# Performance work log

Hardware: AMD Instinct MI355X
Metric: run time of the kernel (lower is better)

Reference implementation:

```python
import jax, jax.numpy as jnp
import numpy as np

N, CH, H, W = 8, 256, 64, 64
M, K = 4, 256
CG = CH // M  # per-group input channels


def setup_inputs() -> dict:
    key = jax.random.key(0)
    k1, k2 = jax.random.split(key)
    x = jax.random.normal(k1, (N, CH, H, W), dtype=jnp.float32)
    # grouped conv1x1 weight: [m, k, c_g]  (torch layout is [m*k, c_g, 1, 1])
    w = jax.random.normal(k2, (M, K, CG), dtype=jnp.float32) / np.float32(np.sqrt(CG))
    return {"x": x, "w": w}


def reference(x, w):
    n, c, h, wd = x.shape
    m, k, cg = w.shape
    # grouped 1x1 conv == per-group matmul over channels
    xg = x.reshape(n, m, cg, h, wd)
    logit5 = jnp.einsum('nmchw,mkc->nmhwk', xg, w)  # [n, m, h, w, k]
    # OneHotCategoricalStraightThrough.rsample():
    # hard one-hot sample + (probs - stop_grad(probs))
    probs = jax.nn.softmax(logit5, axis=-1)
    idx = jax.random.categorical(jax.random.key(42), logit5, axis=-1)  # [n, m, h, w]
    one_hot = jax.nn.one_hot(idx, k, dtype=logit5.dtype)
    quantized = jax.lax.stop_gradient(one_hot) + probs - jax.lax.stop_gradient(probs)
    code = jnp.argmax(quantized, axis=-1)  # [n, m, h, w]
    q_out = jnp.transpose(quantized, (0, 1, 4, 2, 3)).reshape(n, m * k, h, wd)
    logit = jnp.transpose(logit5, (0, 1, 4, 2, 3)).reshape(n, m * k, h, wd)
    return q_out, code, logit
```

## Files before the change

### kernel.cpp

```cpp
#include <hip/hip_runtime.h>
#include <stdint.h>

#define CODE_OFF  33554432u
#define LOGIT_OFF 33685504u

typedef __attribute__((address_space(1))) const void g_void;
typedef __attribute__((address_space(3))) void l_void;

__device__ __forceinline__ uint32_t rotl32(uint32_t x, int r) {
  return (x << r) | (x >> (32 - r));
}

__device__ __forceinline__ uint32_t tf32_part(uint32_t i) {
  const uint32_t ks1 = 42u;
  const uint32_t ks2 = 0x1BD11BDAu ^ 42u;
  uint32_t x0 = 0u;
  uint32_t x1 = i + ks1;
#define R4(a,b,c,d) \
  x0 += x1; x1 = rotl32(x1,(a)); x1 ^= x0; \
  x0 += x1; x1 = rotl32(x1,(b)); x1 ^= x0; \
  x0 += x1; x1 = rotl32(x1,(c)); x1 ^= x0; \
  x0 += x1; x1 = rotl32(x1,(d)); x1 ^= x0;
  R4(13,15,26,6)   x0 += ks1; x1 += ks2 + 1u;
  R4(17,29,16,24)  x0 += ks2; x1 += 2u;
  R4(13,15,26,6)               x1 += ks1 + 3u;
  R4(17,29,16,24)  x0 += ks1; x1 += ks2 + 4u;
  R4(13,15,26,6)   x0 += ks2; x1 += 5u;
#undef R4
  return x0 ^ x1;
}

__device__ __forceinline__ float bits_to_gumbel(uint32_t bits) {
  uint32_t fb = (bits >> 9) | 0x3f800000u;
  float f = __uint_as_float(fb) - 1.0f;
  float u = (f > 0.0f) ? f : 1.17549435e-38f;
  return -logf(-logf(u));
}

__global__ __launch_bounds__(256, 4)
void mcq_kernel(const float* __restrict__ x, const float* __restrict__ w,
                float* __restrict__ out) {
  __shared__ __align__(16) float x_lds[2048];
  __shared__ __align__(16) float w_lds[4096];

  const int tid = threadIdx.x;
  const int tx = tid & 7;
  const int ty = tid >> 3;
  const int half = tx >> 2;
  const int px = tx & 3;
  const int bid = blockIdx.x;
  const int nm = bid >> 8;
  const int tile = bid & 255;
  const int hw0 = tile * 16;
  const int n = nm >> 2;
  const int m = nm & 3;

  float* q_out = out;
  float* code_out = out + CODE_OFF;
  float* logit_out = out + LOGIT_OFF;

  {
    const float* xA = x + (size_t)(n * 256 + m * 64) * 4096 + hw0;
    const float* xB = xA + (size_t)4 * 256 * 4096;
#pragma unroll
    for (int it = 0; it < 2; ++it) {
      int idx = it * 256 + tid;
      int c = idx >> 3;
      int hs = (idx >> 2) & 1;
      int ck = idx & 3;
      const float* src = (hs ? xB : xA) + (size_t)c * 4096 + ck * 4;
      float* dst = x_lds + ((it * 256 + (tid & ~63)) << 2);
      __builtin_amdgcn_global_load_lds((g_void*)src, (l_void*)dst, 16, 0, 0);
    }
  }

  const float* wrow = w + (size_t)m * 256 * 64;
  float4 wr0, wr1;
  {
    const float* wk = wrow + tid * 64;
    wr0 = *(const float4*)(wk + 0);
    wr1 = *(const float4*)(wk + 4);
    w_lds[0 * 256 + tid] = wr0.x; w_lds[1 * 256 + tid] = wr0.y;
    w_lds[2 * 256 + tid] = wr0.z; w_lds[3 * 256 + tid] = wr0.w;
    w_lds[4 * 256 + tid] = wr1.x; w_lds[5 * 256 + tid] = wr1.y;
    w_lds[6 * 256 + tid] = wr1.z; w_lds[7 * 256 + tid] = wr1.w;
  }
  __syncthreads();

  float acc0[8], acc1[8], acc2[8], acc3[8];
  float gmb0[8], gmb1[8], gmb2[8], gmb3[8];
#pragma unroll
  for (int i = 0; i < 8; ++i) acc0[i] = acc1[i] = acc2[i] = acc3[i] = 0.0f;

  const uint32_t base0 = ((uint32_t)((nm + 16 * half) * 4096 + hw0 + 4 * px)) << 8;

#pragma unroll
  for (int chunk = 0; chunk < 8; ++chunk) {
    if (chunk < 7) {
      const float* wk = wrow + tid * 64 + (chunk + 1) * 8;
      wr0 = *(const float4*)(wk + 0);
      wr1 = *(const float4*)(wk + 4);
    }
    {
      const uint32_t k = (uint32_t)((chunk >> 2) * 128 + ty * 4 + (chunk & 3));
      uint32_t b0 = tf32_part(base0 + 0u * 256u + k);
      uint32_t b1 = tf32_part(base0 + 1u * 256u + k);
      uint32_t b2 = tf32_part(base0 + 2u * 256u + k);
      uint32_t b3 = tf32_part(base0 + 3u * 256u + k);
      gmb0[chunk] = bits_to_gumbel(b0);
      gmb1[chunk] = bits_to_gumbel(b1);
      gmb2[chunk] = bits_to_gumbel(b2);
      gmb3[chunk] = bits_to_gumbel(b3);
    }
    const int rb = (chunk & 1) * 2048;
#pragma unroll
    for (int cc = 0; cc < 8; ++cc) {
      int c = chunk * 8 + cc;
      float4 xv = *(const float4*)&x_lds[c * 32 + half * 16 + px * 4];
      float wv[8];
      *(float4*)&wv[0] = *(const float4*)&w_lds[rb + cc * 256 +   0 + ty * 4];
      *(float4*)&wv[4] = *(const float4*)&w_lds[rb + cc * 256 + 128 + ty * 4];
#pragma unroll
      for (int jd = 0; jd < 8; ++jd) {
        float wkv = wv[jd];
        acc0[jd] += xv.x * wkv;
        acc1[jd] += xv.y * wkv;
        acc2[jd] += xv.z * wkv;
        acc3[jd] += xv.w * wkv;
      }
    }
    if (chunk < 7) {
      const int wb = ((chunk + 1) & 1) * 2048;
      w_lds[wb + 0 * 256 + tid] = wr0.x; w_lds[wb + 1 * 256 + tid] = wr0.y;
      w_lds[wb + 2 * 256 + tid] = wr0.z; w_lds[wb + 3 * 256 + tid] = wr0.w;
      w_lds[wb + 4 * 256 + tid] = wr1.x; w_lds[wb + 5 * 256 + tid] = wr1.y;
      w_lds[wb + 6 * 256 + tid] = wr1.z; w_lds[wb + 7 * 256 + tid] = wr1.w;
      __syncthreads();
    }
  }

  float best0 = -3.4e38f, best1 = -3.4e38f, best2 = -3.4e38f, best3 = -3.4e38f;
  int i0 = 0, i1 = 0, i2 = 0, i3 = 0;
  const size_t row_off = (size_t)hw0 + 4 * px;
#pragma unroll
  for (int jd = 0; jd < 8; ++jd) {
    int k = (jd >> 2) * 128 + ty * 4 + (jd & 3);
    size_t off = (size_t)((nm + 16 * half) * 256 + k) * 4096 + row_off;
    *(float4*)(logit_out + off) = make_float4(acc0[jd], acc1[jd], acc2[jd], acc3[jd]);
    float v0 = gmb0[jd] + acc0[jd];
    float v1 = gmb1[jd] + acc1[jd];
    float v2 = gmb2[jd] + acc2[jd];
    float v3 = gmb3[jd] + acc3[jd];
    if (v0 > best0) { best0 = v0; i0 = k; }
    if (v1 > best1) { best1 = v1; i1 = k; }
    if (v2 > best2) { best2 = v2; i2 = k; }
    if (v3 > best3) { best3 = v3; i3 = k; }
  }

  __syncthreads();
  float* red_val = x_lds;
  int* red_idx = (int*)w_lds;
  {
    int slot = half * 16 + px * 4;
    red_val[(slot + 0) * 33 + ty] = best0;  red_idx[(slot + 0) * 33 + ty] = i0;
    red_val[(slot + 1) * 33 + ty] = best1;  red_idx[(slot + 1) * 33 + ty] = i1;
    red_val[(slot + 2) * 33 + ty] = best2;  red_idx[(slot + 2) * 33 + ty] = i2;
    red_val[(slot + 3) * 33 + ty] = best3;  red_idx[(slot + 3) * 33 + ty] = i3;
  }
  __syncthreads();
  int* idx_final = (int*)(x_lds + 1088);
  if (tid < 32) {
    float bv = -3.4e38f; int bi = 0x7fffffff;
#pragma unroll
    for (int t2 = 0; t2 < 32; ++t2) {
      float v = red_val[tid * 33 + t2];
      int ix = red_idx[tid * 33 + t2];
      if (v > bv || (v == bv && ix < bi)) { bv = v; bi = ix; }
    }
    idx_final[tid] = bi;
    int h = tid >> 4;
    int pos = tid & 15;
    code_out[(size_t)(nm + 16 * h) * 4096 + hw0 + pos] = (float)bi;
  }
  __syncthreads();

  const int f0 = idx_final[half * 16 + px * 4 + 0];
  const int f1 = idx_final[half * 16 + px * 4 + 1];
  const int f2 = idx_final[half * 16 + px * 4 + 2];
  const int f3 = idx_final[half * 16 + px * 4 + 3];
#pragma unroll
  for (int jd = 0; jd < 8; ++jd) {
    int k = (jd >> 2) * 128 + ty * 4 + (jd & 3);
    size_t off = (size_t)((nm + 16 * half) * 256 + k) * 4096 + row_off;
    *(float4*)(q_out + off) = make_float4(k == f0 ? 1.0f : 0.0f, k == f1 ? 1.0f : 0.0f,
                                          k == f2 ? 1.0f : 0.0f, k == f3 ? 1.0f : 0.0f);
  }
}

extern "C" void kernel_launch(void* const* d_in, const int* in_sizes, int n_in,
                              void* d_out, int out_size, void* d_ws, size_t ws_size,
                              hipStream_t stream) {
  const float* x = (const float*)d_in[0];
  const float* w = (const float*)d_in[1];
  float* out = (float*)d_out;
  mcq_kernel<<<dim3(4096), dim3(256), 0, stream>>>(x, w, out);
}
```

Measured before the change: 382.7 us.

## Split each block to one plane, doubling grid and halving per-thread tile

Each block now handles a single (n,m) plane instead of two, so the grid doubles to 8192 blocks and each thread computes a 4x4 tile instead of 4x8. The x tile in LDS is halved, Gumbel noise per thread is halved, and the argmax reduction becomes a two-stage 16-slot reduction over 64 threads per pixel. The goal is lower register pressure and more parallelism to hide memory latency in this store-bound kernel. The cost is that every weight slice is loaded and transposed into LDS twice as often overall, and there are extra barriers.

Result: slower. 406.4 us (+6.2%).

```diff
diff --git a/kernel.cpp b/kernel.cpp
--- a/kernel.cpp
+++ b/kernel.cpp
@@ -40,38 +40,29 @@
 __global__ __launch_bounds__(256, 4)
 void mcq_kernel(const float* __restrict__ x, const float* __restrict__ w,
                 float* __restrict__ out) {
-  __shared__ __align__(16) float x_lds[2048];
+  __shared__ __align__(16) float x_lds[1024];
   __shared__ __align__(16) float w_lds[4096];
 
   const int tid = threadIdx.x;
-  const int tx = tid & 7;
-  const int ty = tid >> 3;
-  const int half = tx >> 2;
-  const int px = tx & 3;
+  const int px = tid & 3;
+  const int ty = tid >> 2;
   const int bid = blockIdx.x;
-  const int nm = bid >> 8;
+  const int nm = bid >> 9;
+  const int half = (bid >> 8) & 1;
   const int tile = bid & 255;
   const int hw0 = tile * 16;
-  const int n = nm >> 2;
   const int m = nm & 3;
+  const int plane = nm + 16 * half;
 
   float* q_out = out;
   float* code_out = out + CODE_OFF;
   float* logit_out = out + LOGIT_OFF;
 
   {
-    const float* xA = x + (size_t)(n * 256 + m * 64) * 4096 + hw0;
-    const float* xB = xA + (size_t)4 * 256 * 4096;
-#pragma unroll
-    for (int it = 0; it < 2; ++it) {
-      int idx = it * 256 + tid;
-      int c = idx >> 3;
-      int hs = (idx >> 2) & 1;
-      int ck = idx & 3;
-      const float* src = (hs ? xB : xA) + (size_t)c * 4096 + ck * 4;
-      float* dst = x_lds + ((it * 256 + (tid & ~63)) << 2);
-      __builtin_amdgcn_global_load_lds((g_void*)src, (l_void*)dst, 16, 0, 0);
-    }
+    const float* xbase = x + (size_t)plane * 262144 + hw0;
+    const float* src = xbase + (size_t)(tid >> 2) * 4096 + (tid & 3) * 4;
+    float* dst = x_lds + ((tid & ~63) << 2);
+    __builtin_amdgcn_global_load_lds((g_void*)src, (l_void*)dst, 16, 0, 0);
   }
 
   const float* wrow = w + (size_t)m * 256 * 64;
@@ -87,12 +78,13 @@
   }
   __syncthreads();
 
-  float acc0[8], acc1[8], acc2[8], acc3[8];
-  float gmb0[8], gmb1[8], gmb2[8], gmb3[8];
-#pragma unroll
-  for (int i = 0; i < 8; ++i) acc0[i] = acc1[i] = acc2[i] = acc3[i] = 0.0f;
-
-  const uint32_t base0 = ((uint32_t)((nm + 16 * half) * 4096 + hw0 + 4 * px)) << 8;
+  float acc[4][4], gmb[4][4];
+#pragma unroll
+  for (int p = 0; p < 4; ++p)
+#pragma unroll
+    for (int jd = 0; jd < 4; ++jd) acc[p][jd] = 0.0f;
+
+  const uint32_t base0 = ((uint32_t)(plane * 4096 + hw0 + 4 * px)) << 8;
 
 #pragma unroll
   for (int chunk = 0; chunk < 8; ++chunk) {
@@ -102,35 +94,29 @@
       wr1 = *(const float4*)(wk + 4);
     }
     {
-      const uint32_t k = (uint32_t)((chunk >> 2) * 128 + ty * 4 + (chunk & 3));
-      uint32_t b0 = tf32_part(base0 + 0u * 256u + k);
-      uint32_t b1 = tf32_part(base0 + 1u * 256u + k);
-      uint32_t b2 = tf32_part(base0 + 2u * 256u + k);
-      uint32_t b3 = tf32_part(base0 + 3u * 256u + k);
-      gmb0[chunk] = bits_to_gumbel(b0);
-      gmb1[chunk] = bits_to_gumbel(b1);
-      gmb2[chunk] = bits_to_gumbel(b2);
-      gmb3[chunk] = bits_to_gumbel(b3);
-    }
-    const int rb = (chunk & 1) * 2048;
+#pragma unroll
+      for (int i = 0; i < 2; ++i) {
+        const int d = chunk * 2 + i;
+        const int p = d >> 2, jd = d & 3;
+        const uint32_t k = (uint32_t)(ty * 4 + jd);
+        gmb[p][jd] = bits_to_gumbel(tf32_part(base0 + (uint32_t)p * 256u + k));
+      }
+    }
+    const int rb = (chunk & 1) << 11;
 #pragma unroll
     for (int cc = 0; cc < 8; ++cc) {
       int c = chunk * 8 + cc;
-      float4 xv = *(const float4*)&x_lds[c * 32 + half * 16 + px * 4];
-      float wv[8];
-      *(float4*)&wv[0] = *(const float4*)&w_lds[rb + cc * 256 +   0 + ty * 4];
-      *(float4*)&wv[4] = *(const float4*)&w_lds[rb + cc * 256 + 128 + ty * 4];
-#pragma unroll
-      for (int jd = 0; jd < 8; ++jd) {
-        float wkv = wv[jd];
-        acc0[jd] += xv.x * wkv;
-        acc1[jd] += xv.y * wkv;
-        acc2[jd] += xv.z * wkv;
-        acc3[jd] += xv.w * wkv;
-      }
+      float4 xv = *(const float4*)&x_lds[c * 16 + px * 4];
+      float4 wv = *(const float4*)&w_lds[rb + cc * 256 + ty * 4];
+      float xa[4] = {xv.x, xv.y, xv.z, xv.w};
+      float wa[4] = {wv.x, wv.y, wv.z, wv.w};
+#pragma unroll
+      for (int p = 0; p < 4; ++p)
+#pragma unroll
+        for (int jd = 0; jd < 4; ++jd) acc[p][jd] += xa[p] * wa[jd];
     }
     if (chunk < 7) {
-      const int wb = ((chunk + 1) & 1) * 2048;
+      const int wb = ((chunk + 1) & 1) << 11;
       w_lds[wb + 0 * 256 + tid] = wr0.x; w_lds[wb + 1 * 256 + tid] = wr0.y;
       w_lds[wb + 2 * 256 + tid] = wr0.z; w_lds[wb + 3 * 256 + tid] = wr0.w;
       w_lds[wb + 4 * 256 + tid] = wr1.x; w_lds[wb + 5 * 256 + tid] = wr1.y;
@@ -139,59 +125,68 @@
     }
   }
 
-  float best0 = -3.4e38f, best1 = -3.4e38f, best2 = -3.4e38f, best3 = -3.4e38f;
-  int i0 = 0, i1 = 0, i2 = 0, i3 = 0;
+  float best[4]; int ib[4];
+#pragma unroll
+  for (int p = 0; p < 4; ++p) { best[p] = -3.4e38f; ib[p] = 0; }
   const size_t row_off = (size_t)hw0 + 4 * px;
 #pragma unroll
-  for (int jd = 0; jd < 8; ++jd) {
-    int k = (jd >> 2) * 128 + ty * 4 + (jd & 3);
-    size_t off = (size_t)((nm + 16 * half) * 256 + k) * 4096 + row_off;
-    *(float4*)(logit_out + off) = make_float4(acc0[jd], acc1[jd], acc2[jd], acc3[jd]);
-    float v0 = gmb0[jd] + acc0[jd];
-    float v1 = gmb1[jd] + acc1[jd];
-    float v2 = gmb2[jd] + acc2[jd];
-    float v3 = gmb3[jd] + acc3[jd];
-    if (v0 > best0) { best0 = v0; i0 = k; }
-    if (v1 > best1) { best1 = v1; i1 = k; }
-    if (v2 > best2) { best2 = v2; i2 = k; }
-    if (v3 > best3) { best3 = v3; i3 = k; }
-  }
-
-  __syncthreads();
-  float* red_val = x_lds;
-  int* red_idx = (int*)w_lds;
-  {
-    int slot = half * 16 + px * 4;
-    red_val[(slot + 0) * 33 + ty] = best0;  red_idx[(slot + 0) * 33 + ty] = i0;
-    red_val[(slot + 1) * 33 + ty] = best1;  red_idx[(slot + 1) * 33 + ty] = i1;
-    red_val[(slot + 2) * 33 + ty] = best2;  red_idx[(slot + 2) * 33 + ty] = i2;
-    red_val[(slot + 3) * 33 + ty] = best3;  red_idx[(slot + 3) * 33 + ty] = i3;
-  }
-  __syncthreads();
-  int* idx_final = (int*)(x_lds + 1088);
-  if (tid < 32) {
+  for (int jd = 0; jd < 4; ++jd) {
+    int k = ty * 4 + jd;
+    size_t off = ((size_t)(plane * 256 + k)) * 4096 + row_off;
+    *(float4*)(logit_out + off) =
+        make_float4(acc[0][jd], acc[1][jd], acc[2][jd], acc[3][jd]);
+#pragma unroll
+    for (int p = 0; p < 4; ++p) {
+      float v = gmb[p][jd] + acc[p][jd];
+      if (v > best[p]) { best[p] = v; ib[p] = k; }
+    }
+  }
+
+  __syncthreads();
+  float* red_val = w_lds;
+  int* red_idx = (int*)(w_lds + 1056);
+#pragma unroll
+  for (int p = 0; p < 4; ++p) {
+    int slot = px * 4 + p;
+    red_val[slot * 65 + ty] = best[p];
+    red_idx[slot * 65 + ty] = ib[p];
+  }
+  __syncthreads();
+  float* pv = w_lds + 2112;
+  int* pi = (int*)(w_lds + 2176);
+  if (tid < 64) {
+    int slot = tid >> 2, q = tid & 3;
     float bv = -3.4e38f; int bi = 0x7fffffff;
 #pragma unroll
-    for (int t2 = 0; t2 < 32; ++t2) {
-      float v = red_val[tid * 33 + t2];
-      int ix = red_idx[tid * 33 + t2];
+    for (int t = 0; t < 16; ++t) {
+      float v = red_val[slot * 65 + q * 16 + t];
+      int ix = red_idx[slot * 65 + q * 16 + t];
       if (v > bv || (v == bv && ix < bi)) { bv = v; bi = ix; }
     }
+    pv[slot * 4 + q] = bv; pi[slot * 4 + q] = bi;
+  }
+  __syncthreads();
+  int* idx_final = (int*)x_lds;
+  if (tid < 16) {
+    float bv = -3.4e38f; int bi = 0x7fffffff;
+#pragma unroll
+    for (int q = 0; q < 4; ++q) {
+      float v = pv[tid * 4 + q]; int ix = pi[tid * 4 + q];
+      if (v > bv || (v == bv && ix < bi)) { bv = v; bi = ix; }
+    }
     idx_final[tid] = bi;
-    int h = tid >> 4;
-    int pos = tid & 15;
-    code_out[(size_t)(nm + 16 * h) * 4096 + hw0 + pos] = (float)bi;
-  }
-  __syncthreads();
-
-  const int f0 = idx_final[half * 16 + px * 4 + 0];
-  const int f1 = idx_final[half * 16 + px * 4 + 1];
-  const int f2 = idx_final[half * 16 + px * 4 + 2];
-  const int f3 = idx_final[half * 16 + px * 4 + 3];
-#pragma unroll
-  for (int jd = 0; jd < 8; ++jd) {
-    int k = (jd >> 2) * 128 + ty * 4 + (jd & 3);
-    size_t off = (size_t)((nm + 16 * half) * 256 + k) * 4096 + row_off;
+    code_out[(size_t)plane * 4096 + hw0 + tid] = (float)bi;
+  }
+  __syncthreads();
+
+  const int f0 = idx_final[px * 4 + 0];
+  const int f1 = idx_final[px * 4 + 1];
+  const int f2 = idx_final[px * 4 + 2];
+  const int f3 = idx_final[px * 4 + 3];
+#pragma unroll
+  for (int jd = 0; jd < 4; ++jd) {
+    int k = ty * 4 + jd;
+    size_t off = ((size_t)(plane * 256 + k)) * 4096 + row_off;
     *(float4*)(q_out + off) = make_float4(k == f0 ? 1.0f : 0.0f, k == f1 ? 1.0f : 0.0f,
                                           k == f2 ? 1.0f : 0.0f, k == f3 ? 1.0f : 0.0f);
   }
@@ -203,5 +198,5 @@
   const float* x = (const float*)d_in[0];
   const float* w = (const float*)d_in[1];
   float* out = (float*)d_out;
-  mcq_kernel<<<dim3(4096), dim3(256), 0, stream>>>(x, w, out);
-}
+  mcq_kernel<<<dim3(8192), dim3(256), 0, stream>>>(x, w, out);
+}
```
